# Performance work log

Measured on AMD Instinct MI355X. Metric: run time of the kernel, lower is better.

Reference implementation:

```python
import jax, jax.numpy as jnp
import numpy as np

GROUPS = 16
EPS = 1e-6


def conv1x1(x, w, b):
    # x: (B,C,N,K), w: (O,C), b: (O,)
    return jnp.einsum('oc,bcnk->bonk', w, x) + b[None, :, None, None]


def group_norm(x, gamma, beta):
    # GroupNorm(16, C, eps=1e-6, affine=True) over (C/g, N, K) per sample
    B, C, N, K = x.shape
    xg = x.reshape(B, GROUPS, C // GROUPS, N, K)
    mu = xg.mean(axis=(2, 3, 4), keepdims=True)
    var = xg.var(axis=(2, 3, 4), keepdims=True)
    xn = ((xg - mu) * jax.lax.rsqrt(var + EPS)).reshape(B, C, N, K)
    return xn * gamma[None, :, None, None] + beta[None, :, None, None]


def _gather_nbrs(x, idx):
    # x: (B,C,N), idx: (B,N,K) -> (B,C,N,K)
    return jax.vmap(lambda xb, ib: xb[:, ib])(x, idx)


def lse(coords_t, feats, idx, dist, w, b, g, bt):
    # LocalSpatialEncoding: coords_t (B,3,N), feats (B,C,N,1)
    nbr_coords = _gather_nbrs(coords_t, idx)                       # (B,3,N,K)
    ctr_coords = jnp.broadcast_to(coords_t[..., None], nbr_coords.shape)
    concat = jnp.concatenate(
        [ctr_coords, nbr_coords, ctr_coords - nbr_coords, dist[:, None]], axis=1)  # (B,10,N,K)
    enc = jax.nn.relu(group_norm(conv1x1(concat, w, b), g, bt))    # (B,C,N,K)
    nbr_feats = _gather_nbrs(feats[..., 0], idx)                   # (B,C,N,K)
    return jnp.concatenate([enc, nbr_feats], axis=1)               # (B,2C,N,K)


def attentive_pool(x, w, b, g, bt):
    # mean over K, then SharedMLP with GN+ReLU -> (B,O,N,1)
    m = x.mean(axis=-1, keepdims=True)
    return jax.nn.relu(group_norm(conv1x1(m, w, b), g, bt))


def setup_inputs() -> dict:
    B, N, K, D_IN, D_OUT = 2, 32768, 16, 72, 64
    H = D_OUT // 2  # 32
    key = jax.random.key(0)
    ks = jax.random.split(key, 24)

    def w(k, o, i):
        return jax.random.normal(k, (o, i), jnp.float32) * (1.0 / np.sqrt(i))

    inp = {
        'coords': jax.random.normal(ks[0], (B, N, 3), jnp.float32),
        'features': jax.random.normal(ks[1], (B, D_IN, N, 1), jnp.float32),
        'idx': jax.random.randint(ks[2], (B, N, K), 0, N, jnp.int32),
        'dist': jax.random.uniform(ks[3], (B, N, K), jnp.float32),
        # mlp1: d_in -> d_out//2, LeakyReLU(0.2)
        'w_mlp1': w(ks[4], H, D_IN), 'b_mlp1': jnp.zeros((H,), jnp.float32),
        # lse1 mlp: 10 -> H, GN+ReLU
        'w_lse1': w(ks[5], H, 10), 'b_lse1': jnp.zeros((H,), jnp.float32),
        'g_lse1': jnp.ones((H,), jnp.float32), 'bt_lse1': jnp.zeros((H,), jnp.float32),
        # pool1: d_out -> H, GN+ReLU
        'w_pool1': w(ks[6], H, D_OUT), 'b_pool1': jnp.zeros((H,), jnp.float32),
        'g_pool1': jnp.ones((H,), jnp.float32), 'bt_pool1': jnp.zeros((H,), jnp.float32),
        # lse2 mlp: 10 -> H
        'w_lse2': w(ks[7], H, 10), 'b_lse2': jnp.zeros((H,), jnp.float32),
        'g_lse2': jnp.ones((H,), jnp.float32), 'bt_lse2': jnp.zeros((H,), jnp.float32),
        # pool2: d_out -> d_out
        'w_pool2': w(ks[8], D_OUT, D_OUT), 'b_pool2': jnp.zeros((D_OUT,), jnp.float32),
        'g_pool2': jnp.ones((D_OUT,), jnp.float32), 'bt_pool2': jnp.zeros((D_OUT,), jnp.float32),
        # mlp2: d_out -> 2*d_out (no bn, no act)
        'w_mlp2': w(ks[9], 2 * D_OUT, D_OUT), 'b_mlp2': jnp.zeros((2 * D_OUT,), jnp.float32),
        # shortcut: d_in -> 2*d_out, GN, no act
        'w_sc': w(ks[10], 2 * D_OUT, D_IN), 'b_sc': jnp.zeros((2 * D_OUT,), jnp.float32),
        'g_sc': jnp.ones((2 * D_OUT,), jnp.float32), 'bt_sc': jnp.zeros((2 * D_OUT,), jnp.float32),
    }
    return inp


def reference(coords, features, idx, dist,
              w_mlp1, b_mlp1,
              w_lse1, b_lse1, g_lse1, bt_lse1,
              w_pool1, b_pool1, g_pool1, bt_pool1,
              w_lse2, b_lse2, g_lse2, bt_lse2,
              w_pool2, b_pool2, g_pool2, bt_pool2,
              w_mlp2, b_mlp2,
              w_sc, b_sc, g_sc, bt_sc):
    coords_t = coords.transpose(0, 2, 1)                        # (B,3,N)
    x = jax.nn.leaky_relu(conv1x1(features, w_mlp1, b_mlp1), 0.2)   # (B,32,N,1)
    x = lse(coords_t, x, idx, dist, w_lse1, b_lse1, g_lse1, bt_lse1)  # (B,64,N,K)
    x = attentive_pool(x, w_pool1, b_pool1, g_pool1, bt_pool1)        # (B,32,N,1)
    x = lse(coords_t, x, idx, dist, w_lse2, b_lse2, g_lse2, bt_lse2)  # (B,64,N,K)
    x = attentive_pool(x, w_pool2, b_pool2, g_pool2, bt_pool2)        # (B,64,N,1)
    main = conv1x1(x, w_mlp2, b_mlp2)                                 # (B,128,N,1)
    sc = group_norm(conv1x1(features, w_sc, b_sc), g_sc, bt_sc)       # (B,128,N,1)
    return jax.nn.leaky_relu(main + sc, 0.01)
```

## Files before the change

### kernel.cpp

```cpp
#include <hip/hip_runtime.h>

#define NN 32768
#define GEPS 1e-6f

__device__ __forceinline__ float wredsum(float v){
  v += __shfl_xor(v, 32); v += __shfl_xor(v, 16); v += __shfl_xor(v, 8);
  v += __shfl_xor(v, 4);  v += __shfl_xor(v, 2);  v += __shfl_xor(v, 1);
  return v;
}
__device__ __forceinline__ float eredsum(float v){
  v += __shfl_xor(v, 8); v += __shfl_xor(v, 16); v += __shfl_xor(v, 32);
  return v;
}
__device__ __forceinline__ float ecomb(float v){
  v += __shfl_xor(v, 1); v += __shfl_xor(v, 2); v += __shfl_xor(v, 4);
  return v;
}

__global__ void __launch_bounds__(256) f0_prep(
    const float* __restrict__ w_mlp1, const float* __restrict__ b_mlp1,
    const float* __restrict__ w_sc,   const float* __restrict__ b_sc,
    const float* __restrict__ w_pool1,const float* __restrict__ w_pool2,
    float* __restrict__ WallT, float* __restrict__ ball,
    float* __restrict__ wp1T,  float* __restrict__ wp2T)
{
  const int t0 = blockIdx.x*256 + threadIdx.x;
  const int stride = gridDim.x*256;
  for (int u=t0; u<72*160; u+=stride){
    int i = u/160, o = u - i*160;
    WallT[u] = (o < 128) ? w_sc[o*72+i] : w_mlp1[(o-128)*72+i];
  }
  for (int u=t0; u<160; u+=stride)
    ball[u] = (u < 128) ? b_sc[u] : b_mlp1[u-128];
  for (int u=t0; u<64*32; u+=stride){ int c=u>>5, o=u&31; wp1T[u] = w_pool1[o*64+c]; }
  for (int u=t0; u<64*64; u+=stride){ int c=u>>6, o=u&63; wp2T[u] = w_pool2[o*64+c]; }
}

__global__ void __launch_bounds__(256,2) k0_mlp1_scstats(
    const float* __restrict__ feat, const float* __restrict__ WallT,
    const float* __restrict__ ball,
    float* __restrict__ X1, float* __restrict__ scS, float* __restrict__ scQ)
{
  __shared__ float xl[72][128];
  __shared__ float wl[72*32];
  __shared__ float ssl[128], sql[128];
  const int tid = threadIdx.x, lane = tid & 63;
  const int wid = __builtin_amdgcn_readfirstlane(tid >> 6);
  const int b   = __builtin_amdgcn_readfirstlane((int)blockIdx.x >> 8);
  const int n0  = ((int)blockIdx.x & 255) << 7;
  const int p0  = lane*2;

  for (int u=tid; u<72*128; u+=256){
    int c = u>>7, j = u&127;
    xl[c][j] = feat[(size_t)(b*72+c)*NN + n0 + j];
  }

#pragma unroll 1
  for (int pass=0; pass<5; ++pass){
    __syncthreads();
    for (int u=tid; u<2304; u+=256){
      int i = u>>5, c = u&31;
      wl[u] = WallT[i*160 + pass*32 + c];
    }
    __syncthreads();

    const int oc = pass*32 + wid*8;
    float a0[8], a1[8];
#pragma unroll
    for (int q=0;q<8;q++){ float bv = ball[oc+q]; a0[q]=bv; a1[q]=bv; }

    const float* wbase = wl + wid*8;
#pragma unroll
    for (int i=0;i<72;i++){
      const float2 x2 = *(const float2*)&xl[i][p0];
      const float4 w0 = *(const float4*)(wbase + i*32);
      const float4 w1 = *(const float4*)(wbase + i*32 + 4);
      a0[0]=fmaf(w0.x,x2.x,a0[0]); a1[0]=fmaf(w0.x,x2.y,a1[0]);
      a0[1]=fmaf(w0.y,x2.x,a0[1]); a1[1]=fmaf(w0.y,x2.y,a1[1]);
      a0[2]=fmaf(w0.z,x2.x,a0[2]); a1[2]=fmaf(w0.z,x2.y,a1[2]);
      a0[3]=fmaf(w0.w,x2.x,a0[3]); a1[3]=fmaf(w0.w,x2.y,a1[3]);
      a0[4]=fmaf(w1.x,x2.x,a0[4]); a1[4]=fmaf(w1.x,x2.y,a1[4]);
      a0[5]=fmaf(w1.y,x2.x,a0[5]); a1[5]=fmaf(w1.y,x2.y,a1[5]);
      a0[6]=fmaf(w1.z,x2.x,a0[6]); a1[6]=fmaf(w1.z,x2.y,a1[6]);
      a0[7]=fmaf(w1.w,x2.x,a0[7]); a1[7]=fmaf(w1.w,x2.y,a1[7]);
    }

    if (pass < 4){
#pragma unroll
      for (int q=0;q<8;q++){
        float s  = wredsum(a0[q]+a1[q]);
        float s2 = wredsum(a0[q]*a0[q] + a1[q]*a1[q]);
        if (lane==0){ ssl[oc+q] = s; sql[oc+q] = s2; }
      }
    } else {
      __syncthreads();
      float* xst = &xl[0][0];
#pragma unroll
      for (int q=0;q<8;q++){
        float v0 = a0[q], v1 = a1[q];
        v0 = v0 > 0.f ? v0 : 0.2f*v0;
        v1 = v1 > 0.f ? v1 : 0.2f*v1;
        float2 t; t.x=v0; t.y=v1;
        *(float2*)&xst[(wid*8+q)*130 + p0] = t;
      }
      __syncthreads();
      float* xb = X1 + ((size_t)b*NN + n0)*32;
#pragma unroll
      for (int r=0;r<4;r++){
        int u = tid + r*256;
        int p = u>>3, c0 = (u&7)*4;
        float4 o;
        o.x = xst[(c0+0)*130+p]; o.y = xst[(c0+1)*130+p];
        o.z = xst[(c0+2)*130+p]; o.w = xst[(c0+3)*130+p];
        *(float4*)(xb + (size_t)p*32 + c0) = o;
      }
    }
  }

  if (tid < 128){
    atomicAdd(&scS[b*128+tid], ssl[tid]);
    atomicAdd(&scQ[b*128+tid], sql[tid]);
  }
}

__global__ void __launch_bounds__(256) k1_vmom(
    const float* __restrict__ coords, const int* __restrict__ idx,
    const float* __restrict__ dist, float* __restrict__ vm)
{
  __shared__ float red[4*65];
  const int tid = threadIdx.x, lane = tid & 63, wid = tid >> 6;
  const int gn = blockIdx.x*256 + tid;
  const int pt = gn >> 2, h = gn & 3;
  const int b = pt >> 15, n = pt & (NN-1);
  const size_t pb = (size_t)b*NN + n;
  const float c0 = coords[pb*3+0], c1 = coords[pb*3+1], c2 = coords[pb*3+2];

  int ja[4]; float da[4];
  {
    int4 j4 = *(const int4*)(idx + pb*16 + h*4);
    float4 d4 = *(const float4*)(dist + pb*16 + h*4);
    ja[0]=j4.x; ja[1]=j4.y; ja[2]=j4.z; ja[3]=j4.w;
    da[0]=d4.x; da[1]=d4.y; da[2]=d4.z; da[3]=d4.w;
  }

  float aS[10], aM[55];
#pragma unroll
  for (int i=0;i<10;i++) aS[i]=0.f;
#pragma unroll
  for (int i=0;i<55;i++) aM[i]=0.f;

#pragma unroll
  for (int k=0;k<4;k++){
    const float* nb = coords + ((size_t)b*NN + ja[k])*3;
    const float n0v=nb[0], n1v=nb[1], n2v=nb[2];
    const float v[10] = {c0,c1,c2,n0v,n1v,n2v,c0-n0v,c1-n1v,c2-n2v,da[k]};
#pragma unroll
    for (int i=0;i<10;i++){
      aS[i] += v[i];
#pragma unroll
      for (int j=i;j<10;j++)
        aM[i*10 - (i*(i-1))/2 + (j-i)] += v[i]*v[j];
    }
  }

#pragma unroll
  for (int i=0;i<10;i++){ float s = wredsum(aS[i]); if (lane==0) red[wid*65+i] = s; }
#pragma unroll
  for (int i=0;i<55;i++){ float s = wredsum(aM[i]); if (lane==0) red[wid*65+10+i] = s; }
  __syncthreads();
  if (tid < 65){
    float s = red[tid] + red[65+tid] + red[130+tid] + red[195+tid];
    const int bb = blockIdx.x >> 9;
    atomicAdd(&vm[bb*65+tid], s);
  }
}

__global__ void f1_fold(
    const float* __restrict__ w_lse1, const float* __restrict__ b_lse1,
    const float* __restrict__ g_lse1, const float* __restrict__ bt_lse1,
    const float* __restrict__ w_lse2, const float* __restrict__ b_lse2,
    const float* __restrict__ g_lse2, const float* __restrict__ bt_lse2,
    const float* __restrict__ vm,
    float* __restrict__ w1p, float* __restrict__ w2p)
{
  const int tid = threadIdx.x;
  const int half = tid >> 6;
  const int u = tid & 63, b = u >> 5, c = u & 31;
  const float* W  = half ? w_lse2  : w_lse1;
  const float* Bv = half ? b_lse2  : b_lse1;
  const float* G  = half ? g_lse2  : g_lse1;
  const float* Bt = half ? bt_lse2 : bt_lse1;
  float wr[10];
#pragma unroll
  for (int i=0;i<10;i++) wr[i] = W[c*10+i];
  const float* S = vm + b*65;
  const float* M = vm + b*65 + 10;
  float P = 0.f;
#pragma unroll
  for (int i=0;i<10;i++) P = fmaf(wr[i], S[i], P);
  float Q = 0.f;
#pragma unroll
  for (int i=0;i<10;i++){
#pragma unroll
    for (int j=i;j<10;j++){
      float m = M[i*10 - (i*(i-1))/2 + (j-i)];
      float t = wr[i]*wr[j]*m;
      Q += (i==j) ? t : 2.f*t;
    }
  }
  const float invNK = 1.f/((float)NN*16.f);
  const float bc = Bv[c];
  float mean = P*invNK + bc;
  float ey2  = (Q + 2.f*bc*P)*invNK + bc*bc;
  float mu = 0.5f*(mean + __shfl_xor(mean,1));
  float e2 = 0.5f*(ey2  + __shfl_xor(ey2, 1));
  float var = e2 - mu*mu;
  float rstd = rsqrtf(var + GEPS);
  float a = G[c]*rstd, d = Bt[c] - mu*a;
  float* out = (half ? w2p : w1p) + (b*32+c)*12;
#pragma unroll
  for (int i=0;i<10;i++) out[i] = wr[i]*a;
  out[10] = bc*a + d;
  out[11] = 0.f;
}

__global__ void __launch_bounds__(256,8) k2_lse1_pool1(
    const float* __restrict__ coords, const int* __restrict__ idx,
    const float* __restrict__ dist, const float* __restrict__ X1,
    const float* __restrict__ w1p, const float* __restrict__ wp1T,
    const float* __restrict__ b_pool1,
    float* __restrict__ Y1, float* __restrict__ p1S, float* __restrict__ p1Q)
{
  __shared__ float mfl[32*66];
  __shared__ float sl[32], ql[32];
  const int tid = threadIdx.x, lane = tid & 63;
  const int e = tid & 7;
  const int pl = tid >> 3;
  if (tid < 32){ sl[tid]=0.f; ql[tid]=0.f; }
  __syncthreads();
  const int b = __builtin_amdgcn_readfirstlane((int)blockIdx.x & 1);
  const int n = (((int)blockIdx.x >> 1) << 5) + pl;
  const size_t pb = (size_t)b*NN + n;
  float* mf = &mfl[pl*66];
  const float s16 = 0.0625f;

  {
    int ja[16];
    const int4* ip = (const int4*)(idx + pb*16);
#pragma unroll
    for (int k4=0;k4<4;k4++){
      int4 j4 = ip[k4];
      ja[k4*4+0]=j4.x; ja[k4*4+1]=j4.y; ja[k4*4+2]=j4.z; ja[k4*4+3]=j4.w;
    }
    float af0=0.f, af1=0.f, af2=0.f, af3=0.f;
    const float* xb = X1 + (size_t)b*NN*32 + e*4;
#pragma unroll 4
    for (int k=0;k<16;k++){
      float4 g = *(const float4*)(xb + (size_t)ja[k]*32);
      af0+=g.x; af1+=g.y; af2+=g.z; af3+=g.w;
    }
    mf[32+e*4+0]=af0*s16; mf[32+e*4+1]=af1*s16;
    mf[32+e*4+2]=af2*s16; mf[32+e*4+3]=af3*s16;
  }

  {
    int2 j2 = *(const int2*)(idx + pb*16 + e*2);
    float2 d2 = *(const float2*)(dist + pb*16 + e*2);
    const float* nb0 = coords + ((size_t)b*NN + j2.x)*3;
    const float* nb1 = coords + ((size_t)b*NN + j2.y)*3;
    const float nx0=nb0[0], ny0=nb0[1], nz0=nb0[2];
    const float nx1=nb1[0], ny1=nb1[1], nz1=nb1[2];
    const float c0=coords[pb*3], c1=coords[pb*3+1], c2=coords[pb*3+2];
    const float* wrow = w1p + (size_t)(b*32)*12;
#pragma unroll 1
    for (int cc=0;cc<4;cc++){
      float ptc[8];
#pragma unroll
      for (int q=0;q<8;q++){
        const float4* r4 = (const float4*)(wrow + (cc*8+q)*12);
        float4 ra=r4[0], rb=r4[1], rc=r4[2];
        const float t0=ra.x+rb.z, t1=ra.y+rb.w, t2=ra.z+rc.x;
        const float u0=ra.w-rb.z, u1=rb.x-rb.w, u2=rb.y-rc.x;
        const float wd=rc.y;
        float cb = rc.z;
        cb = fmaf(t0,c0,cb); cb = fmaf(t1,c1,cb); cb = fmaf(t2,c2,cb);
        float s0 = cb, s1 = cb;
        s0 = fmaf(u0,nx0,s0); s0 = fmaf(u1,ny0,s0); s0 = fmaf(u2,nz0,s0);
        s0 = fmaf(wd,d2.x,s0);
        s1 = fmaf(u0,nx1,s1); s1 = fmaf(u1,ny1,s1); s1 = fmaf(u2,nz1,s1);
        s1 = fmaf(wd,d2.y,s1);
        ptc[q] = fmaxf(s0,0.f) + fmaxf(s1,0.f);
      }
#pragma unroll
      for (int q=0;q<8;q++) ptc[q] = ecomb(ptc[q]);
      if ((e>>1)==cc){
        float v0 = (e&1) ? ptc[4] : ptc[0];
        float v1 = (e&1) ? ptc[5] : ptc[1];
        float v2 = (e&1) ? ptc[6] : ptc[2];
        float v3 = (e&1) ? ptc[7] : ptc[3];
        mf[e*4+0]=v0*s16; mf[e*4+1]=v1*s16;
        mf[e*4+2]=v2*s16; mf[e*4+3]=v3*s16;
      }
    }
  }
  __syncthreads();

  const int o0 = e*4;
  float yac[4];
  {
    const float4 b0 = *(const float4*)(b_pool1 + o0);
    yac[0]=b0.x; yac[1]=b0.y; yac[2]=b0.z; yac[3]=b0.w;
  }
#pragma unroll 4
  for (int c=0;c<64;c++){
    const float mc = mf[c];
    const float4 w0 = *(const float4*)(wp1T + c*32 + o0);
    yac[0]=fmaf(w0.x,mc,yac[0]); yac[1]=fmaf(w0.y,mc,yac[1]);
    yac[2]=fmaf(w0.z,mc,yac[2]); yac[3]=fmaf(w0.w,mc,yac[3]);
  }
  {
    float4 r0; r0.x=yac[0]; r0.y=yac[1]; r0.z=yac[2]; r0.w=yac[3];
    *(float4*)(Y1 + pb*32 + o0) = r0;
  }
#pragma unroll
  for (int q=0;q<4;q++){
    float s  = eredsum(yac[q]);
    float s2 = eredsum(yac[q]*yac[q]);
    if (lane < 8){ atomicAdd(&sl[o0+q], s); atomicAdd(&ql[o0+q], s2); }
  }
  __syncthreads();
  if (tid<32){ atomicAdd(&p1S[b*32+tid], sl[tid]); atomicAdd(&p1Q[b*32+tid], ql[tid]); }
}

__global__ void __launch_bounds__(256) f2_apply_pool1(
    float* __restrict__ Y1, const float* __restrict__ p1S, const float* __restrict__ p1Q,
    const float* __restrict__ g, const float* __restrict__ bt)
{
  __shared__ float al[32], dl[32];
  const int tid = threadIdx.x;
  const int b = blockIdx.x >> 10;
  if (tid < 32){
    float s = p1S[b*32+tid], q = p1Q[b*32+tid];
    s += __shfl_xor(s,1); q += __shfl_xor(q,1);
    const float inv = 1.f/(2.f*(float)NN);
    float mu = s*inv, e2 = q*inv, var = e2-mu*mu;
    float rstd = rsqrtf(var + GEPS);
    float a = g[tid]*rstd;
    al[tid] = a; dl[tid] = bt[tid] - mu*a;
  }
  __syncthreads();
  const size_t e4 = (size_t)blockIdx.x*256 + tid;
  float4* Y = (float4*)Y1;
  float4 v = Y[e4];
  const int c0 = ((int)(e4 & 7))*4;
  v.x = fmaxf(fmaf(v.x, al[c0+0], dl[c0+0]), 0.f);
  v.y = fmaxf(fmaf(v.y, al[c0+1], dl[c0+1]), 0.f);
  v.z = fmaxf(fmaf(v.z, al[c0+2], dl[c0+2]), 0.f);
  v.w = fmaxf(fmaf(v.w, al[c0+3], dl[c0+3]), 0.f);
  Y[e4] = v;
}

__global__ void __launch_bounds__(256,8) k4_lse2_pool2(
    const float* __restrict__ coords, const int* __restrict__ idx,
    const float* __restrict__ dist, const float* __restrict__ Y1,
    const float* __restrict__ w2p, const float* __restrict__ wp2T,
    const float* __restrict__ b_pool2,
    float* __restrict__ Y2T, float* __restrict__ p2S, float* __restrict__ p2Q)
{
  __shared__ float mfl[32*66];
  __shared__ float sl[64], ql[64];
  const int tid = threadIdx.x, lane = tid & 63;
  const int e = tid & 7;
  const int pl = tid >> 3;
  if (tid < 64){ sl[tid]=0.f; ql[tid]=0.f; }
  __syncthreads();
  const int b = __builtin_amdgcn_readfirstlane((int)blockIdx.x & 1);
  const int n0g = (((int)blockIdx.x >> 1) << 5);
  const int n = n0g + pl;
  const size_t pb = (size_t)b*NN + n;
  float* mf = &mfl[pl*66];
  const float s16 = 0.0625f;

  {
    int ja[16];
    const int4* ip = (const int4*)(idx + pb*16);
#pragma unroll
    for (int k4=0;k4<4;k4++){
      int4 j4 = ip[k4];
      ja[k4*4+0]=j4.x; ja[k4*4+1]=j4.y; ja[k4*4+2]=j4.z; ja[k4*4+3]=j4.w;
    }
    float af0=0.f, af1=0.f, af2=0.f, af3=0.f;
    const float* yb = Y1 + (size_t)b*NN*32 + e*4;
#pragma unroll 4
    for (int k=0;k<16;k++){
      float4 g = *(const float4*)(yb + (size_t)ja[k]*32);
      af0+=g.x; af1+=g.y; af2+=g.z; af3+=g.w;
    }
    mf[32+e*4+0]=af0*s16; mf[32+e*4+1]=af1*s16;
    mf[32+e*4+2]=af2*s16; mf[32+e*4+3]=af3*s16;
  }

  {
    int2 j2 = *(const int2*)(idx + pb*16 + e*2);
    float2 d2 = *(const float2*)(dist + pb*16 + e*2);
    const float* nb0 = coords + ((size_t)b*NN + j2.x)*3;
    const float* nb1 = coords + ((size_t)b*NN + j2.y)*3;
    const float nx0=nb0[0], ny0=nb0[1], nz0=nb0[2];
    const float nx1=nb1[0], ny1=nb1[1], nz1=nb1[2];
    const float c0=coords[pb*3], c1=coords[pb*3+1], c2=coords[pb*3+2];
    const float* wrow = w2p + (size_t)(b*32)*12;
#pragma unroll 1
    for (int cc=0;cc<4;cc++){
      float ptc[8];
#pragma unroll
      for (int q=0;q<8;q++){
        const float4* r4 = (const float4*)(wrow + (cc*8+q)*12);
        float4 ra=r4[0], rb=r4[1], rc=r4[2];
        const float t0=ra.x+rb.z, t1=ra.y+rb.w, t2=ra.z+rc.x;
        const float u0=ra.w-rb.z, u1=rb.x-rb.w, u2=rb.y-rc.x;
        const float wd=rc.y;
        float cb = rc.z;
        cb = fmaf(t0,c0,cb); cb = fmaf(t1,c1,cb); cb = fmaf(t2,c2,cb);
        float s0 = cb, s1 = cb;
        s0 = fmaf(u0,nx0,s0); s0 = fmaf(u1,ny0,s0); s0 = fmaf(u2,nz0,s0);
        s0 = fmaf(wd,d2.x,s0);
        s1 = fmaf(u0,nx1,s1); s1 = fmaf(u1,ny1,s1); s1 = fmaf(u2,nz1,s1);
        s1 = fmaf(wd,d2.y,s1);
        ptc[q] = fmaxf(s0,0.f) + fmaxf(s1,0.f);
      }
#pragma unroll
      for (int q=0;q<8;q++) ptc[q] = ecomb(ptc[q]);
      if ((e>>1)==cc){
        float v0 = (e&1) ? ptc[4] : ptc[0];
        float v1 = (e&1) ? ptc[5] : ptc[1];
        float v2 = (e&1) ? ptc[6] : ptc[2];
        float v3 = (e&1) ? ptc[7] : ptc[3];
        mf[e*4+0]=v0*s16; mf[e*4+1]=v1*s16;
        mf[e*4+2]=v2*s16; mf[e*4+3]=v3*s16;
      }
    }
  }
  __syncthreads();

  const int o0 = e*8;
  float yac[8];
  {
    const float4 b0 = *(const float4*)(b_pool2 + o0);
    const float4 b1 = *(const float4*)(b_pool2 + o0 + 4);
    yac[0]=b0.x; yac[1]=b0.y; yac[2]=b0.z; yac[3]=b0.w;
    yac[4]=b1.x; yac[5]=b1.y; yac[6]=b1.z; yac[7]=b1.w;
  }
#pragma unroll 4
  for (int c=0;c<64;c++){
    const float mc = mf[c];
    const float4 w0 = *(const float4*)(wp2T + c*64 + o0);
    const float4 w1 = *(const float4*)(wp2T + c*64 + o0 + 4);
    yac[0]=fmaf(w0.x,mc,yac[0]); yac[1]=fmaf(w0.y,mc,yac[1]);
    yac[2]=fmaf(w0.z,mc,yac[2]); yac[3]=fmaf(w0.w,mc,yac[3]);
    yac[4]=fmaf(w1.x,mc,yac[4]); yac[5]=fmaf(w1.y,mc,yac[5]);
    yac[6]=fmaf(w1.z,mc,yac[6]); yac[7]=fmaf(w1.w,mc,yac[7]);
  }
#pragma unroll
  for (int q=0;q<8;q++){
    float s  = eredsum(yac[q]);
    float s2 = eredsum(yac[q]*yac[q]);
    if (lane < 8){ atomicAdd(&sl[o0+q], s); atomicAdd(&ql[o0+q], s2); }
  }
  __syncthreads();
  float* ldsT = &mfl[0];
#pragma unroll
  for (int o=0;o<8;o++) ldsT[(o0+o)*33 + pl] = yac[o];
  __syncthreads();
#pragma unroll
  for (int r=0;r<8;r++){
    int u = tid + r*256;
    int ch = u >> 5, p = u & 31;
    Y2T[((size_t)(b*64+ch))*NN + n0g + p] = ldsT[ch*33 + p];
  }
  if (tid<64){ atomicAdd(&p2S[b*64+tid], sl[tid]); atomicAdd(&p2Q[b*64+tid], ql[tid]); }
}

__global__ void f3a_affines(
    const float* __restrict__ scS, const float* __restrict__ scQ,
    const float* __restrict__ g_sc, const float* __restrict__ bt_sc,
    const float* __restrict__ b_sc, const float* __restrict__ b_mlp2,
    const float* __restrict__ p2S, const float* __restrict__ p2Q,
    const float* __restrict__ g_p2, const float* __restrict__ bt_p2,
    float* __restrict__ ascT, float* __restrict__ cstF,
    float* __restrict__ a2F, float* __restrict__ d2F)
{
  const int tid = threadIdx.x;
  if (tid < 256){
    const int b = tid >> 7, c = tid & 127;
    float s = scS[b*128+c], q = scQ[b*128+c];
    s += __shfl_xor(s,1); q += __shfl_xor(q,1);
    s += __shfl_xor(s,2); q += __shfl_xor(q,2);
    s += __shfl_xor(s,4); q += __shfl_xor(q,4);
    const float inv = 1.f/(8.f*(float)NN);
    float mu = s*inv, e2 = q*inv, var = e2-mu*mu;
    float rstd = rsqrtf(var + GEPS);
    float a = g_sc[c]*rstd;
    ascT[tid] = a;
    cstF[tid] = b_mlp2[c] + a*b_sc[c] + (bt_sc[c] - mu*a);
  } else {
    const int t = tid - 256;
    const int b = t >> 6, c = t & 63;
    float s = p2S[b*64+c], q = p2Q[b*64+c];
    s += __shfl_xor(s,1); q += __shfl_xor(q,1);
    s += __shfl_xor(s,2); q += __shfl_xor(q,2);
    const float inv = 1.f/(4.f*(float)NN);
    float mu = s*inv, e2 = q*inv, var = e2-mu*mu;
    float rstd = rsqrtf(var + GEPS);
    float a = g_p2[c]*rstd;
    a2F[t] = a; d2F[t] = bt_p2[c] - mu*a;
  }
}

__global__ void __launch_bounds__(256) f3b_wcomb(
    const float* __restrict__ w_mlp2, const float* __restrict__ w_sc,
    const float* __restrict__ ascT, float* __restrict__ Wcomb)
{
  const int t0 = blockIdx.x*256 + threadIdx.x;
  const int stride = gridDim.x*256;
  for (int u=t0; u<2*136*128; u+=stride){
    int bb = u / 17408;
    int rr = u - bb*17408;
    int i = rr >> 7, o = rr & 127;
    Wcomb[u] = (i < 64) ? w_mlp2[o*64+i]
                        : w_sc[o*72 + (i-64)] * ascT[bb*128+o];
  }
}

__global__ void __launch_bounds__(256,3) k6_final(
    const float* __restrict__ feat, const float* __restrict__ Y2T,
    const float* __restrict__ Wcomb, const float* __restrict__ cstF,
    const float* __restrict__ a2F, const float* __restrict__ d2F,
    float* __restrict__ out)
{
  __shared__ float xl[68*128];
  __shared__ float wl[68*64];
  const int tid = threadIdx.x, lane = tid & 63;
  const int wid = __builtin_amdgcn_readfirstlane(tid >> 6);
  const int g   = __builtin_amdgcn_readfirstlane((int)blockIdx.x >> 9);
  const int b   = __builtin_amdgcn_readfirstlane(((int)blockIdx.x >> 8) & 1);
  const int n0  = ((int)blockIdx.x & 255) << 7;
  const int p0  = lane*2;

  float acc[2][2][8];
#pragma unroll
  for (int ps=0; ps<2; ps++){
#pragma unroll
    for (int q=0;q<8;q++){
      float bv = cstF[b*128 + g*64 + ps*32 + wid*8 + q];
      acc[ps][0][q]=bv; acc[ps][1][q]=bv;
    }
  }

  const float* Wb = Wcomb + b*17408 + g*64;
#pragma unroll 1
  for (int half=0; half<2; ++half){
    __syncthreads();
    for (int u=tid; u<68*128; u+=256){
      int row = u>>7, j = u&127;
      int r = half*68 + row;
      float v;
      if (r < 64){
        float y = Y2T[(size_t)(b*64+r)*NN + n0 + j];
        v = fmaxf(fmaf(y, a2F[b*64+r], d2F[b*64+r]), 0.f);
      } else {
        v = feat[(size_t)(b*72 + (r-64))*NN + n0 + j];
      }
      xl[u] = v;
    }
    for (int u=tid; u<68*64; u+=256){
      int i = u>>6, c = u&63;
      wl[u] = Wb[(size_t)(half*68+i)*128 + c];
    }
    __syncthreads();

    const float* wbase = wl + wid*8;
#pragma unroll 2
    for (int i=0;i<68;i++){
      const float2 x2 = *(const float2*)&xl[i*128 + p0];
#pragma unroll
      for (int ps=0; ps<2; ps++){
        const float4 wA = *(const float4*)(wbase + i*64 + ps*32);
        const float4 wB = *(const float4*)(wbase + i*64 + ps*32 + 4);
        const float wv[8] = {wA.x,wA.y,wA.z,wA.w,wB.x,wB.y,wB.z,wB.w};
#pragma unroll
        for (int q=0;q<8;q++){
          acc[ps][0][q] = fmaf(wv[q], x2.x, acc[ps][0][q]);
          acc[ps][1][q] = fmaf(wv[q], x2.y, acc[ps][1][q]);
        }
      }
    }
  }

#pragma unroll
  for (int ps=0; ps<2; ps++){
#pragma unroll
    for (int q=0;q<8;q++){
      const int ch = b*128 + g*64 + ps*32 + wid*8 + q;
      float v0 = acc[ps][0][q], v1 = acc[ps][1][q];
      float2 r;
      r.x = v0 > 0.f ? v0 : 0.01f*v0;
      r.y = v1 > 0.f ? v1 : 0.01f*v1;
      *(float2*)(out + (size_t)ch*NN + n0 + p0) = r;
    }
  }
}

extern "C" void kernel_launch(void* const* d_in, const int* in_sizes, int n_in,
                              void* d_out, int out_size, void* d_ws, size_t ws_size,
                              hipStream_t stream) {
  (void)in_sizes; (void)n_in; (void)out_size; (void)ws_size;
  const float* coords  = (const float*)d_in[0];
  const float* feats   = (const float*)d_in[1];
  const int*   idx     = (const int*)  d_in[2];
  const float* dist    = (const float*)d_in[3];
  const float* w_mlp1  = (const float*)d_in[4];
  const float* b_mlp1  = (const float*)d_in[5];
  const float* w_lse1  = (const float*)d_in[6];
  const float* b_lse1  = (const float*)d_in[7];
  const float* g_lse1  = (const float*)d_in[8];
  const float* bt_lse1 = (const float*)d_in[9];
  const float* w_pool1 = (const float*)d_in[10];
  const float* b_pool1 = (const float*)d_in[11];
  const float* g_pool1 = (const float*)d_in[12];
  const float* bt_pool1= (const float*)d_in[13];
  const float* w_lse2  = (const float*)d_in[14];
  const float* b_lse2  = (const float*)d_in[15];
  const float* g_lse2  = (const float*)d_in[16];
  const float* bt_lse2 = (const float*)d_in[17];
  const float* w_pool2 = (const float*)d_in[18];
  const float* b_pool2 = (const float*)d_in[19];
  const float* g_pool2 = (const float*)d_in[20];
  const float* bt_pool2= (const float*)d_in[21];
  const float* w_mlp2  = (const float*)d_in[22];
  const float* b_mlp2  = (const float*)d_in[23];
  const float* w_sc    = (const float*)d_in[24];
  const float* b_sc    = (const float*)d_in[25];
  const float* g_sc    = (const float*)d_in[26];
  const float* bt_sc   = (const float*)d_in[27];

  float* ws   = (float*)d_ws;
  float* scS  = ws;
  float* scQ  = ws + 256;
  float* vm   = ws + 512;
  float* p1S  = ws + 704;
  float* p1Q  = ws + 768;
  float* p2S  = ws + 832;
  float* p2Q  = ws + 960;
  float* w1p  = ws + 1280;
  float* w2p  = ws + 2048;
  float* wp1T = ws + 2816;
  float* wp2T = ws + 4864;
  float* ball = ws + 8960;
  float* cstF = ws + 9120;
  float* a2F  = ws + 9376;
  float* d2F  = ws + 9504;
  float* ascT = ws + 9632;
  float* WallT= ws + 9984;
  float* Wcomb= ws + 21504;
  float* X1   = ws + 57344;
  float* Y1   = X1 + (size_t)2*NN*32;
  float* Y2T  = Y1 + (size_t)2*NN*32;

  hipMemsetAsync(d_ws, 0, 1088*sizeof(float), stream);

  f0_prep<<<32,256,0,stream>>>(w_mlp1,b_mlp1,w_sc,b_sc,w_pool1,w_pool2,
                               WallT,ball,wp1T,wp2T);
  k0_mlp1_scstats<<<512,256,0,stream>>>(feats, WallT, ball, X1, scS, scQ);
  k1_vmom<<<1024,256,0,stream>>>(coords, idx, dist, vm);
  f1_fold<<<1,128,0,stream>>>(w_lse1,b_lse1,g_lse1,bt_lse1,
                              w_lse2,b_lse2,g_lse2,bt_lse2,
                              vm, w1p, w2p);
  k2_lse1_pool1<<<2048,256,0,stream>>>(coords, idx, dist, X1, w1p, wp1T, b_pool1,
                                       Y1, p1S, p1Q);
  f2_apply_pool1<<<2048,256,0,stream>>>(Y1, p1S, p1Q, g_pool1, bt_pool1);
  k4_lse2_pool2<<<2048,256,0,stream>>>(coords, idx, dist, Y1, w2p, wp2T, b_pool2,
                                       Y2T, p2S, p2Q);
  f3a_affines<<<1,384,0,stream>>>(scS,scQ,g_sc,bt_sc,b_sc,b_mlp2,
                                  p2S,p2Q,g_pool2,bt_pool2, ascT,cstF,a2F,d2F);
  f3b_wcomb<<<64,256,0,stream>>>(w_mlp2, w_sc, ascT, Wcomb);
  k6_final<<<1024,256,0,stream>>>(feats, Y2T, Wcomb, cstF, a2F, d2F, (float*)d_out);
}
```

Baseline: 277.6 us.

## Retile final GEMM kernel to compute all 128 output channels per block

The final fused mlp2+shortcut GEMM kernel now computes all 128 output channels per block, where before the channel dimension was split across two groups of blocks that each reloaded the same input tile. Each thread keeps an 8x8 register tile (8 points by 8 channels), and the K dimension is staged through LDS in four chunks of 34 rows. This removes the duplicated reads of Y2T and features and raises FMAs per LDS load. In exchange it uses more accumulator registers, lowers the occupancy hint to 2 and halves the grid to 512 blocks.

```diff
diff --git a/kernel.cpp b/kernel.cpp
--- a/kernel.cpp
+++ b/kernel.cpp
@@ -531,38 +531,35 @@
   }
 }
 
-__global__ void __launch_bounds__(256,3) k6_final(
+__global__ void __launch_bounds__(256,2) k6_final(
     const float* __restrict__ feat, const float* __restrict__ Y2T,
     const float* __restrict__ Wcomb, const float* __restrict__ cstF,
     const float* __restrict__ a2F, const float* __restrict__ d2F,
     float* __restrict__ out)
 {
-  __shared__ float xl[68*128];
-  __shared__ float wl[68*64];
-  const int tid = threadIdx.x, lane = tid & 63;
-  const int wid = __builtin_amdgcn_readfirstlane(tid >> 6);
-  const int g   = __builtin_amdgcn_readfirstlane((int)blockIdx.x >> 9);
-  const int b   = __builtin_amdgcn_readfirstlane(((int)blockIdx.x >> 8) & 1);
-  const int n0  = ((int)blockIdx.x & 255) << 7;
-  const int p0  = lane*2;
-
-  float acc[2][2][8];
-#pragma unroll
-  for (int ps=0; ps<2; ps++){
-#pragma unroll
-    for (int q=0;q<8;q++){
-      float bv = cstF[b*128 + g*64 + ps*32 + wid*8 + q];
-      acc[ps][0][q]=bv; acc[ps][1][q]=bv;
-    }
-  }
-
-  const float* Wb = Wcomb + b*17408 + g*64;
+  __shared__ float xl[34*128];
+  __shared__ float wl[34*128];
+  const int tid = threadIdx.x;
+  const int tc = tid & 15;
+  const int tp = tid >> 4;
+  const int b  = __builtin_amdgcn_readfirstlane((int)blockIdx.x >> 8);
+  const int n0 = ((int)blockIdx.x & 255) << 7;
+
+  float acc[8][8];
+#pragma unroll
+  for (int q=0;q<8;q++){
+    float bv = cstF[b*128 + tc*8 + q];
+#pragma unroll
+    for (int p=0;p<8;p++) acc[p][q] = bv;
+  }
+
+  const float* Wb = Wcomb + b*17408;
 #pragma unroll 1
-  for (int half=0; half<2; ++half){
+  for (int kk=0; kk<4; ++kk){
     __syncthreads();
-    for (int u=tid; u<68*128; u+=256){
+    for (int u=tid; u<34*128; u+=256){
       int row = u>>7, j = u&127;
-      int r = half*68 + row;
+      int r = kk*34 + row;
       float v;
       if (r < 64){
         float y = Y2T[(size_t)(b*64+r)*NN + n0 + j];
@@ -572,41 +569,44 @@
       }
       xl[u] = v;
     }
-    for (int u=tid; u<68*64; u+=256){
-      int i = u>>6, c = u&63;
-      wl[u] = Wb[(size_t)(half*68+i)*128 + c];
+    for (int u=tid; u<34*128; u+=256){
+      int row = u>>7, c = u&127;
+      wl[u] = Wb[(size_t)(kk*34+row)*128 + c];
     }
     __syncthreads();
 
-    const float* wbase = wl + wid*8;
 #pragma unroll 2
-    for (int i=0;i<68;i++){
-      const float2 x2 = *(const float2*)&xl[i*128 + p0];
-#pragma unroll
-      for (int ps=0; ps<2; ps++){
-        const float4 wA = *(const float4*)(wbase + i*64 + ps*32);
-        const float4 wB = *(const float4*)(wbase + i*64 + ps*32 + 4);
-        const float wv[8] = {wA.x,wA.y,wA.z,wA.w,wB.x,wB.y,wB.z,wB.w};
-#pragma unroll
-        for (int q=0;q<8;q++){
-          acc[ps][0][q] = fmaf(wv[q], x2.x, acc[ps][0][q]);
-          acc[ps][1][q] = fmaf(wv[q], x2.y, acc[ps][1][q]);
-        }
-      }
-    }
-  }
-
-#pragma unroll
-  for (int ps=0; ps<2; ps++){
-#pragma unroll
-    for (int q=0;q<8;q++){
-      const int ch = b*128 + g*64 + ps*32 + wid*8 + q;
-      float v0 = acc[ps][0][q], v1 = acc[ps][1][q];
-      float2 r;
-      r.x = v0 > 0.f ? v0 : 0.01f*v0;
-      r.y = v1 > 0.f ? v1 : 0.01f*v1;
-      *(float2*)(out + (size_t)ch*NN + n0 + p0) = r;
-    }
+    for (int i=0;i<34;i++){
+      const float4 xa = *(const float4*)&xl[i*128 + tp*8];
+      const float4 xb = *(const float4*)&xl[i*128 + tp*8 + 4];
+      const float4 wa = *(const float4*)&wl[i*128 + tc*8];
+      const float4 wb = *(const float4*)&wl[i*128 + tc*8 + 4];
+      const float xs[8] = {xa.x,xa.y,xa.z,xa.w,xb.x,xb.y,xb.z,xb.w};
+      const float wv[8] = {wa.x,wa.y,wa.z,wa.w,wb.x,wb.y,wb.z,wb.w};
+#pragma unroll
+      for (int p=0;p<8;p++)
+#pragma unroll
+        for (int q=0;q<8;q++)
+          acc[p][q] = fmaf(wv[q], xs[p], acc[p][q]);
+    }
+  }
+
+#pragma unroll
+  for (int q=0;q<8;q++){
+    const int ch = b*128 + tc*8 + q;
+    float4 r0, r1;
+    float v;
+    v = acc[0][q]; r0.x = v>0.f? v : 0.01f*v;
+    v = acc[1][q]; r0.y = v>0.f? v : 0.01f*v;
+    v = acc[2][q]; r0.z = v>0.f? v : 0.01f*v;
+    v = acc[3][q]; r0.w = v>0.f? v : 0.01f*v;
+    v = acc[4][q]; r1.x = v>0.f? v : 0.01f*v;
+    v = acc[5][q]; r1.y = v>0.f? v : 0.01f*v;
+    v = acc[6][q]; r1.z = v>0.f? v : 0.01f*v;
+    v = acc[7][q]; r1.w = v>0.f? v : 0.01f*v;
+    float* ob = out + (size_t)ch*NN + n0 + tp*8;
+    *(float4*)(ob)     = r0;
+    *(float4*)(ob + 4) = r1;
   }
 }
 
@@ -683,5 +683,5 @@
   f3a_affines<<<1,384,0,stream>>>(scS,scQ,g_sc,bt_sc,b_sc,b_mlp2,
                                   p2S,p2Q,g_pool2,bt_pool2, ascT,cstF,a2F,d2F);
   f3b_wcomb<<<64,256,0,stream>>>(w_mlp2, w_sc, ascT, Wcomb);
-  k6_final<<<1024,256,0,stream>>>(feats, Y2T, Wcomb, cstF, a2F, d2F, (float*)d_out);
-}
+  k6_final<<<512,256,0,stream>>>(feats, Y2T, Wcomb, cstF, a2F, d2F, (float*)d_out);
+}
```

Measured after the change: 259.1 us. 1.07x faster.
